# Kernel tuning notes

Hardware: AMD Instinct MI355X
Metric: run time of the kernel (lower is better)

Reference implementation:

```python
import jax, jax.numpy as jnp
import numpy as np

STATE_LEN = 128
SEQ_LEN = 2048  # middle segment length; total T = SEQ_LEN + 2*STATE_LEN = 2304


def _l2norm(t):
    # matches torch F.normalize(p=2, dim=-1, eps=1e-12)
    n = jnp.sqrt(jnp.sum(t * t, axis=-1, keepdims=True))
    return t / jnp.maximum(n, 1e-12)


def setup_inputs() -> dict:
    key = jax.random.key(0)
    ks = jax.random.split(key, 8)
    B, D, H, dk, dv = 1, 1024, 16, 64, 64
    T = SEQ_LEN + 2 * STATE_LEN
    x = jax.random.normal(ks[0], (B, T, D), dtype=jnp.float32)
    w = lambda k, do: jax.random.normal(k, (H, D, do), dtype=jnp.float32) * 0.02
    return {
        "x": x,
        "Wq": w(ks[1], dk),
        "Wk": w(ks[2], dk),
        "Wv": w(ks[3], dv),
        "Wq_state": w(ks[4], dk),
        "Wk_state": w(ks[5], dk),
        "Wv_state": w(ks[6], dv),
        "scaling_factor": jnp.full((H,), 1.0 / np.sqrt(dk), dtype=jnp.float32),
    }


def reference(x, Wq, Wk, Wv, Wq_state, Wk_state, Wv_state, scaling_factor):
    sl, seq = STATE_LEN, SEQ_LEN
    # extract_state: [start_state | sequence | end_state]
    x0 = x[:, :sl]
    xm = x[:, sl:sl + seq]
    x1 = x[:, sl + seq:]

    proj = lambda t, W: jnp.einsum('bsd,hdk->bhsk', t, W)  # StackedLinear, no bias

    q = jnp.concatenate([_l2norm(proj(x0, Wq_state)), _l2norm(proj(xm, Wq)), _l2norm(proj(x1, Wq_state))], axis=2)
    k = jnp.concatenate([_l2norm(proj(x0, Wk_state)), _l2norm(proj(xm, Wk)), _l2norm(proj(x1, Wk_state))], axis=2)
    v = jnp.concatenate([_l2norm(proj(x0, Wv_state)), _l2norm(proj(xm, Wv)), _l2norm(proj(x1, Wv_state))], axis=2)

    T = q.shape[2]
    row = jnp.arange(T)[:, None]
    col = jnp.arange(T)[None, :]
    allowed = col <= row  # causal (tril, diagonal=0)
    # end-state rows may not attend to start-state cols (attn_bias[..., seq+sl:seq+2sl, :sl] = 0 before log)
    allowed = allowed & ~((row >= sl + seq) & (col < sl))
    mask = jnp.where(allowed, 0.0, -jnp.inf).astype(q.dtype)  # log of 0/1 tril

    # per-head learnable scale applied to q@k^T, then additive mask, softmax, @v
    scores = jnp.einsum('bhqd,bhkd->bhqk', q, k) * scaling_factor[None, :, None, None] + mask
    att = jax.nn.softmax(scores, axis=-1)
    return jnp.einsum('bhqk,bhkd->bhqd', att, v)
```

## Files before the change

kernel.cpp:

```cpp
#include <hip/hip_runtime.h>
#include <hip/hip_bf16.h>

#define T_TOT 2304
#define DDIM  1024
#define NH    16
#define DK    64
#define SLEN  128
#define SEQ   2048

typedef __bf16 bf16x8 __attribute__((ext_vector_type(8)));
typedef __bf16 bf16x4 __attribute__((ext_vector_type(4)));
typedef float  f32x4  __attribute__((ext_vector_type(4)));

__device__ __forceinline__ void async_copy16(const void* gsrc, void* ldst) {
  __builtin_amdgcn_global_load_lds(
      (const __attribute__((address_space(1))) void*)gsrc,
      (__attribute__((address_space(3))) void*)ldst, 16, 0, 0);
}

__device__ __forceinline__ void lds_barrier() {
  __asm__ volatile("s_waitcnt lgkmcnt(0)\n\ts_barrier" ::: "memory");
}

__global__ __launch_bounds__(256) void convert_kernel(
    const float* __restrict__ x,
    const float* __restrict__ Wq, const float* __restrict__ Wk,
    const float* __restrict__ Wv, const float* __restrict__ Wqs,
    const float* __restrict__ Wks, const float* __restrict__ Wvs,
    __bf16* __restrict__ xb, __bf16* __restrict__ Wt) {
  const int b = blockIdx.x;
  const int tid = threadIdx.x;
  if (b < 576) {
    const float4* xin = (const float4*)x;
#pragma unroll
    for (int it = 0; it < 4; ++it) {
      int idx4 = b * 1024 + it * 256 + tid;
      float4 v = xin[idx4];
      bf16x4 o;
      o[0] = (__bf16)v.x; o[1] = (__bf16)v.y; o[2] = (__bf16)v.z; o[3] = (__bf16)v.w;
      *(bf16x4*)(xb + (size_t)idx4 * 4) = o;
    }
    return;
  }
  __shared__ float tile[64 * 65];
  const int wb = b - 576;
  const int m  = wb >> 8;
  const int rem = wb & 255;
  const int h  = rem >> 4;
  const int dt = rem & 15;
  const int d0 = dt * 64;
  const float* Wsrc = (m == 0 ? Wq : m == 1 ? Wk : m == 2 ? Wv
                      : m == 3 ? Wqs : m == 4 ? Wks : Wvs) + (size_t)h * (DDIM * DK);
#pragma unroll
  for (int rr = 0; rr < 4; ++rr) {
    int drow = rr * 16 + (tid >> 4);
    int nc   = (tid & 15) * 4;
    float4 v = *(const float4*)(Wsrc + (size_t)(d0 + drow) * DK + nc);
    tile[(nc + 0) * 65 + drow] = v.x;
    tile[(nc + 1) * 65 + drow] = v.y;
    tile[(nc + 2) * 65 + drow] = v.z;
    tile[(nc + 3) * 65 + drow] = v.w;
  }
  __syncthreads();
  {
    int n  = tid >> 2;
    int rg = (tid & 3) * 16;
    __bf16* dst = Wt + (((size_t)(m * NH + h)) * DK + n) * DDIM + d0 + rg;
    bf16x8 o0, o1;
#pragma unroll
    for (int e = 0; e < 8; e++) o0[e] = (__bf16)tile[n * 65 + rg + e];
#pragma unroll
    for (int e = 0; e < 8; e++) o1[e] = (__bf16)tile[n * 65 + rg + 8 + e];
    *(bf16x8*)dst = o0;
    *(bf16x8*)(dst + 8) = o1;
  }
}

__global__ __launch_bounds__(256) void proj_kernel(
    const __bf16* __restrict__ xb, const __bf16* __restrict__ Wt,
    const float* __restrict__ scal,
    __bf16* __restrict__ qkv, __bf16* __restrict__ vt) {
  const int ntile = blockIdx.x;
  const int rt    = blockIdx.y;
  const int which = blockIdx.z;
  const int r0    = rt * 64;
  const int m     = (rt < 2 || rt >= 34) ? which + 3 : which;

  __shared__ __bf16 Xs[64 * 64];
  __shared__ __bf16 Wsh[128 * 64];

  const int tid  = threadIdx.x;
  const int wave = tid >> 6, lane = tid & 63;
  const int quad = lane >> 4, lc = lane & 15;
  const int wr   = wave >> 1, wc = wave & 1;
  const int h    = ntile * 2 + wc;

  const __bf16* Wbase = Wt + ((size_t)m * NH) * (DK * DDIM) + (size_t)(ntile * 128) * DDIM;

  const f32x4 fz = {0.f, 0.f, 0.f, 0.f};
  f32x4 acc[2][4];
#pragma unroll
  for (int i = 0; i < 2; i++)
#pragma unroll
    for (int j = 0; j < 4; j++) acc[i][j] = fz;

  for (int k0 = 0; k0 < DDIM; k0 += 64) {
#pragma unroll
    for (int it = 0; it < 2; ++it) {
      int L = it * 256 + tid;
      int row = L >> 3, c = (L & 7) ^ (row & 7);
      async_copy16(xb + (size_t)(r0 + row) * DDIM + k0 + c * 8,
                   (char*)Xs + (size_t)(it * 256 + wave * 64) * 16);
    }
#pragma unroll
    for (int it = 0; it < 4; ++it) {
      int L = it * 256 + tid;
      int row = L >> 3, c = (L & 7) ^ (row & 7);
      async_copy16(Wbase + (size_t)row * DDIM + k0 + c * 8,
                   (char*)Wsh + (size_t)(it * 256 + wave * 64) * 16);
    }
    __syncthreads();
#pragma unroll
    for (int kk = 0; kk < 2; kk++) {
      bf16x8 afr[2], bfr[4];
#pragma unroll
      for (int i = 0; i < 2; i++) {
        int row = wr * 32 + i * 16 + lc;
        int ch  = (kk * 4 + quad) ^ (row & 7);
        afr[i] = *(const bf16x8*)(Xs + (row * 8 + ch) * 8);
      }
#pragma unroll
      for (int j = 0; j < 4; j++) {
        int row = wc * 64 + j * 16 + lc;
        int ch  = (kk * 4 + quad) ^ (row & 7);
        bfr[j] = *(const bf16x8*)(Wsh + (row * 8 + ch) * 8);
      }
#pragma unroll
      for (int i = 0; i < 2; i++)
#pragma unroll
        for (int j = 0; j < 4; j++)
          acc[i][j] = __builtin_amdgcn_mfma_f32_16x16x32_bf16(afr[i], bfr[j], acc[i][j], 0, 0, 0);
    }
    __syncthreads();
  }

  const float qscale = (which == 0) ? scal[h] * 1.44269504088896f : 1.0f;
  float inv4[2][4];
#pragma unroll
  for (int i = 0; i < 2; i++) {
#pragma unroll
    for (int r = 0; r < 4; r++) {
      float s = 0.f;
#pragma unroll
      for (int j = 0; j < 4; j++) { float v = acc[i][j][r]; s += v * v; }
#pragma unroll
      for (int off = 1; off < 16; off <<= 1) s += __shfl_xor(s, off, 64);
      inv4[i][r] = qscale / fmaxf(sqrtf(s), 1e-12f);
    }
  }
  if (which == 2) {
    __bf16* vtp = vt + (size_t)h * (DK * T_TOT);
#pragma unroll
    for (int i = 0; i < 2; i++) {
      int rowbase = r0 + wr * 32 + i * 16 + quad * 4;
#pragma unroll
      for (int j = 0; j < 4; j++) {
        bf16x4 o;
#pragma unroll
        for (int r = 0; r < 4; r++) o[r] = (__bf16)(acc[i][j][r] * inv4[i][r]);
        *(bf16x4*)(vtp + (size_t)(j * 16 + lc) * T_TOT + rowbase) = o;
      }
    }
  } else {
    __bf16* outp = qkv + ((size_t)(which * NH + h)) * ((size_t)T_TOT * DK);
#pragma unroll
    for (int i = 0; i < 2; i++)
#pragma unroll
      for (int r = 0; r < 4; r++) {
        int row = r0 + wr * 32 + i * 16 + quad * 4 + r;
#pragma unroll
        for (int j = 0; j < 4; j++)
          outp[(size_t)row * DK + j * 16 + lc] = (__bf16)(acc[i][j][r] * inv4[i][r]);
      }
  }
}

__global__ __launch_bounds__(256, 3) void attn_kernel(
    const __bf16* __restrict__ qkv, const __bf16* __restrict__ vt,
    float* __restrict__ Opart, float* __restrict__ Lpart) {
  const int b    = blockIdx.x;
  const int h    = b & 15;
  const int rest = b >> 4;
  const int qg   = 35 - (rest >> 1);
  const int si   = rest & 1;
  const int q0b  = qg * 64;
  const int tid  = threadIdx.x;
  const int wave = tid >> 6, lane = tid & 63;
  const int quad = lane >> 4, lc = lane & 15;

  const __bf16* qp = qkv + ((size_t)h) * ((size_t)T_TOT * DK);
  const __bf16* kp = qkv + ((size_t)(NH + h)) * ((size_t)T_TOT * DK);
  const __bf16* vp = vt + (size_t)h * (DK * T_TOT);

  __shared__ __align__(16) char smem[40960];
  __bf16* Ks = (__bf16*)smem;
  __bf16* Vs = (__bf16*)(smem + 16384);
  __bf16* Pw = (__bf16*)(smem + 32768) + wave * 1024;

  bf16x8 qf[2];
#pragma unroll
  for (int kk = 0; kk < 2; kk++)
    qf[kk] = *(const bf16x8*)(qp + (size_t)(q0b + wave * 16 + lc) * DK + kk * 32 + quad * 8);

  const f32x4 fz = {0.f, 0.f, 0.f, 0.f};
  f32x4 acc[4];
#pragma unroll
  for (int dt = 0; dt < 4; dt++) acc[dt] = fz;
  float lp = 0.f;

  const int jsAll = (q0b >= SLEN + SEQ) ? 2 : 0;
  const int n     = qg - jsAll + 1;
  const int half  = (n + 1) >> 1;
  const int j0    = jsAll + (si ? half : 0);
  const int j1    = si ? qg : (jsAll + half - 1);

  auto stage = [&](int j, int bufi) {
    const __bf16* kT = kp + (size_t)j * 64 * DK;
    __bf16* Kd = Ks + bufi * 4096;
    __bf16* Vd = Vs + bufi * 4096;
#pragma unroll
    for (int it = 0; it < 2; ++it) {
      int L = it * 256 + tid;
      int row = L >> 3, c = (L & 7) ^ (row & 7);
      async_copy16(kT + (size_t)row * DK + c * 8,
                   (char*)Kd + (size_t)(it * 256 + wave * 64) * 16);
    }
#pragma unroll
    for (int it = 0; it < 2; ++it) {
      int L = it * 256 + tid;
      int d = L >> 3, c = (L & 7) ^ (d & 7);
      async_copy16(vp + (size_t)d * T_TOT + j * 64 + c * 8,
                   (char*)Vd + (size_t)(it * 256 + wave * 64) * 16);
    }
  };

  int cur = 0;
  if (j0 <= j1) stage(j0, 0);

  for (int j = j0; j <= j1; ++j) {
    __syncthreads();
    if (j < j1) stage(j + 1, cur ^ 1);

    const __bf16* Kc = Ks + cur * 4096;
    const __bf16* Vc = Vs + cur * 4096;

    f32x4 s[4];
#pragma unroll
    for (int kvt = 0; kvt < 4; kvt++) {
      int row = kvt * 16 + lc;
      bf16x8 a0 = *(const bf16x8*)(Kc + (row * 8 + (quad ^ (lc & 7))) * 8);
      bf16x8 a1 = *(const bf16x8*)(Kc + (row * 8 + ((4 + quad) ^ (lc & 7))) * 8);
      f32x4 t = __builtin_amdgcn_mfma_f32_16x16x32_bf16(a0, qf[0], fz, 0, 0, 0);
      s[kvt]  = __builtin_amdgcn_mfma_f32_16x16x32_bf16(a1, qf[1], t, 0, 0, 0);
    }

    const bool diag = (j == qg);
#pragma unroll
    for (int kvt = 0; kvt < 4; kvt++) {
      if (diag) {
#pragma unroll
        for (int r = 0; r < 4; r++)
          if ((kvt * 16 + quad * 4 + r) > (wave * 16 + lc)) s[kvt][r] = -__builtin_inff();
      }
      bf16x4 pb;
#pragma unroll
      for (int r = 0; r < 4; r++) {
        float pe = exp2f(s[kvt][r]);
        lp += pe;
        pb[r] = (__bf16)pe;
      }
      int c = (kvt * 4 + quad) ^ ((lc & 7) << 1);
      *(bf16x4*)(Pw + lc * 64 + c * 4) = pb;
    }

    bf16x8 pB[2];
#pragma unroll
    for (int kk = 0; kk < 2; kk++)
      pB[kk] = *(const bf16x8*)(Pw + lc * 64 + ((kk * 8 + quad * 2) ^ ((lc & 7) << 1)) * 4);
#pragma unroll
    for (int dt = 0; dt < 4; dt++) {
      int row = dt * 16 + lc;
#pragma unroll
      for (int kk = 0; kk < 2; kk++) {
        bf16x8 vA = *(const bf16x8*)(Vc + (row * 8 + ((kk * 4 + quad) ^ (lc & 7))) * 8);
        acc[dt] = __builtin_amdgcn_mfma_f32_16x16x32_bf16(vA, pB[kk], acc[dt], 0, 0, 0);
      }
    }
    cur ^= 1;
  }

  lp += __shfl_xor(lp, 16, 64);
  lp += __shfl_xor(lp, 32, 64);
  if (lane < 16) Lpart[(size_t)b * 64 + wave * 16 + lane] = lp;

  __syncthreads();
  float* Ot = (float*)smem + wave * (16 * 68);
#pragma unroll
  for (int dt = 0; dt < 4; dt++)
#pragma unroll
    for (int r = 0; r < 4; r++)
      Ot[lc * 68 + dt * 16 + quad * 4 + r] = acc[dt][r];

  float* Ob = Opart + (size_t)b * 4096;
  const int q2 = lane >> 2, dsg = (lane & 3) * 16;
#pragma unroll
  for (int g = 0; g < 4; g++) {
    f32x4 v = *(const f32x4*)(&Ot[q2 * 68 + dsg + g * 4]);
    *(f32x4*)(&Ob[(size_t)(wave * 16 + q2) * 64 + dsg + g * 4]) = v;
  }
}

__global__ __launch_bounds__(256) void combine_kernel(
    const float* __restrict__ Opart, const float* __restrict__ Lpart,
    float* __restrict__ out) {
  const int b  = blockIdx.x;
  const int h  = b & 15;
  const int qg = b >> 4;
  const int b0 = (((35 - qg) * 2) << 4) | h;
  const int b1 = b0 + 16;
  const int tid = threadIdx.x;

  __shared__ float invl[64];
  if (tid < 64)
    invl[tid] = 1.0f / (Lpart[(size_t)b0 * 64 + tid] + Lpart[(size_t)b1 * 64 + tid]);
  __syncthreads();

  const float* O0 = Opart + (size_t)b0 * 4096;
  const float* O1 = Opart + (size_t)b1 * 4096;
  float* op = out + ((size_t)h * T_TOT + qg * 64) * DK;
#pragma unroll
  for (int it = 0; it < 4; ++it) {
    int i4 = it * 256 + tid;
    f32x4 a = *(const f32x4*)(&O0[i4 * 4]);
    f32x4 c = *(const f32x4*)(&O1[i4 * 4]);
    float iv = invl[i4 >> 4];
    f32x4 o;
#pragma unroll
    for (int r = 0; r < 4; r++) o[r] = (a[r] + c[r]) * iv;
    *(f32x4*)(&op[i4 * 4]) = o;
  }
}

extern "C" void kernel_launch(void* const* d_in, const int* in_sizes, int n_in,
                              void* d_out, int out_size, void* d_ws, size_t ws_size,
                              hipStream_t stream) {
  const float* x    = (const float*)d_in[0];
  const float* Wq   = (const float*)d_in[1];
  const float* Wk   = (const float*)d_in[2];
  const float* Wv   = (const float*)d_in[3];
  const float* Wqs  = (const float*)d_in[4];
  const float* Wks  = (const float*)d_in[5];
  const float* Wvs  = (const float*)d_in[6];
  const float* scal = (const float*)d_in[7];
  float* out = (float*)d_out;

  char* ws = (char*)d_ws;
  size_t off = 0;
  __bf16* xb    = (__bf16*)(ws + off); off += (size_t)T_TOT * DDIM * 2;
  __bf16* Wt    = (__bf16*)(ws + off); off += (size_t)6 * NH * DK * DDIM * 2;
  __bf16* qkv   = (__bf16*)(ws + off); off += (size_t)2 * NH * T_TOT * DK * 2;
  __bf16* vt    = (__bf16*)(ws + off); off += (size_t)NH * DK * T_TOT * 2;
  float*  Opart = (float*)(ws + off);  off += (size_t)1152 * 4096 * 4;
  float*  Lpart = (float*)(ws + off);

  convert_kernel<<<2112, 256, 0, stream>>>(x, Wq, Wk, Wv, Wqs, Wks, Wvs, xb, Wt);
  proj_kernel<<<dim3(8, 36, 3), 256, 0, stream>>>(xb, Wt, scal, qkv, vt);
  attn_kernel<<<dim3(1152), 256, 0, stream>>>(qkv, vt, Opart, Lpart);
  combine_kernel<<<dim3(576), 256, 0, stream>>>(Opart, Lpart, out);
}
```

Measured before the change: 142.1 us.

## Load projection GEMM operands directly from global memory into registers, dropping LDS staging

The projection kernel stops staging X and W tiles in shared memory through async copies and barriers. Each lane now loads its MFMA fragments straight from global memory into registers, and the k-loop is unrolled by two. This removes LDS traffic and block-wide synchronisation. In exchange, operands shared across waves are fetched redundantly from global memory or cache, and the reads are less coalesced.

```diff
diff --git a/kernel.cpp b/kernel.cpp
--- a/kernel.cpp
+++ b/kernel.cpp
@@ -16,10 +16,6 @@
   __builtin_amdgcn_global_load_lds(
       (const __attribute__((address_space(1))) void*)gsrc,
       (__attribute__((address_space(3))) void*)ldst, 16, 0, 0);
-}
-
-__device__ __forceinline__ void lds_barrier() {
-  __asm__ volatile("s_waitcnt lgkmcnt(0)\n\ts_barrier" ::: "memory");
 }
 
 __global__ __launch_bounds__(256) void convert_kernel(
@@ -86,16 +82,19 @@
   const int r0    = rt * 64;
   const int m     = (rt < 2 || rt >= 34) ? which + 3 : which;
 
-  __shared__ __bf16 Xs[64 * 64];
-  __shared__ __bf16 Wsh[128 * 64];
-
   const int tid  = threadIdx.x;
   const int wave = tid >> 6, lane = tid & 63;
   const int quad = lane >> 4, lc = lane & 15;
   const int wr   = wave >> 1, wc = wave & 1;
   const int h    = ntile * 2 + wc;
 
-  const __bf16* Wbase = Wt + ((size_t)m * NH) * (DK * DDIM) + (size_t)(ntile * 128) * DDIM;
+  const __bf16* xb0 = xb + (size_t)(r0 + wr * 32 + lc) * DDIM + quad * 8;
+  const __bf16* xb1 = xb0 + 16 * DDIM;
+  const __bf16* wb0 = Wt + ((size_t)m * NH) * (DK * DDIM)
+                    + (size_t)(ntile * 128 + wc * 64 + lc) * DDIM + quad * 8;
+  const __bf16* wb1 = wb0 + 16 * DDIM;
+  const __bf16* wb2 = wb0 + 32 * DDIM;
+  const __bf16* wb3 = wb0 + 48 * DDIM;
 
   const f32x4 fz = {0.f, 0.f, 0.f, 0.f};
   f32x4 acc[2][4];
@@ -104,44 +103,25 @@
 #pragma unroll
     for (int j = 0; j < 4; j++) acc[i][j] = fz;
 
+#pragma unroll 2
   for (int k0 = 0; k0 < DDIM; k0 += 64) {
-#pragma unroll
-    for (int it = 0; it < 2; ++it) {
-      int L = it * 256 + tid;
-      int row = L >> 3, c = (L & 7) ^ (row & 7);
-      async_copy16(xb + (size_t)(r0 + row) * DDIM + k0 + c * 8,
-                   (char*)Xs + (size_t)(it * 256 + wave * 64) * 16);
-    }
-#pragma unroll
-    for (int it = 0; it < 4; ++it) {
-      int L = it * 256 + tid;
-      int row = L >> 3, c = (L & 7) ^ (row & 7);
-      async_copy16(Wbase + (size_t)row * DDIM + k0 + c * 8,
-                   (char*)Wsh + (size_t)(it * 256 + wave * 64) * 16);
-    }
-    __syncthreads();
+    bf16x8 afr[2][2], bfr[4][2];
 #pragma unroll
     for (int kk = 0; kk < 2; kk++) {
-      bf16x8 afr[2], bfr[4];
-#pragma unroll
-      for (int i = 0; i < 2; i++) {
-        int row = wr * 32 + i * 16 + lc;
-        int ch  = (kk * 4 + quad) ^ (row & 7);
-        afr[i] = *(const bf16x8*)(Xs + (row * 8 + ch) * 8);
-      }
-#pragma unroll
-      for (int j = 0; j < 4; j++) {
-        int row = wc * 64 + j * 16 + lc;
-        int ch  = (kk * 4 + quad) ^ (row & 7);
-        bfr[j] = *(const bf16x8*)(Wsh + (row * 8 + ch) * 8);
-      }
+      afr[0][kk] = *(const bf16x8*)(xb0 + k0 + kk * 32);
+      afr[1][kk] = *(const bf16x8*)(xb1 + k0 + kk * 32);
+      bfr[0][kk] = *(const bf16x8*)(wb0 + k0 + kk * 32);
+      bfr[1][kk] = *(const bf16x8*)(wb1 + k0 + kk * 32);
+      bfr[2][kk] = *(const bf16x8*)(wb2 + k0 + kk * 32);
+      bfr[3][kk] = *(const bf16x8*)(wb3 + k0 + kk * 32);
+    }
+#pragma unroll
+    for (int kk = 0; kk < 2; kk++)
 #pragma unroll
       for (int i = 0; i < 2; i++)
 #pragma unroll
         for (int j = 0; j < 4; j++)
-          acc[i][j] = __builtin_amdgcn_mfma_f32_16x16x32_bf16(afr[i], bfr[j], acc[i][j], 0, 0, 0);
-    }
-    __syncthreads();
+          acc[i][j] = __builtin_amdgcn_mfma_f32_16x16x32_bf16(afr[i][kk], bfr[j][kk], acc[i][j], 0, 0, 0);
   }
 
   const float qscale = (which == 0) ? scal[h] * 1.44269504088896f : 1.0f;
```

New measurement: 209.8 us. 47.7% more time.

## Process 128-query tiles per block with three-way KV split in attention

Applied to the files above, without the earlier changes.

The attention kernel now handles 128 query rows per block, with each wave owning two 16-row query subtiles. Each staged K/V tile in LDS is therefore reused across twice as many queries, and the KV range is split three ways instead of two. The combine kernel now sums three partials, and waves whose rows lie entirely before a KV tile skip its compute. This raises register use and LDS to 48KB per block under the launch bound of 3, and the causal-diagonal blocks do more masked work.

```diff
diff --git a/kernel.cpp b/kernel.cpp
--- a/kernel.cpp
+++ b/kernel.cpp
@@ -16,10 +16,6 @@
   __builtin_amdgcn_global_load_lds(
       (const __attribute__((address_space(1))) void*)gsrc,
       (__attribute__((address_space(3))) void*)ldst, 16, 0, 0);
-}
-
-__device__ __forceinline__ void lds_barrier() {
-  __asm__ volatile("s_waitcnt lgkmcnt(0)\n\ts_barrier" ::: "memory");
 }
 
 __global__ __launch_bounds__(256) void convert_kernel(
@@ -189,11 +185,11 @@
     const __bf16* __restrict__ qkv, const __bf16* __restrict__ vt,
     float* __restrict__ Opart, float* __restrict__ Lpart) {
   const int b    = blockIdx.x;
-  const int h    = b & 15;
-  const int rest = b >> 4;
-  const int qg   = 35 - (rest >> 1);
-  const int si   = rest & 1;
-  const int q0b  = qg * 64;
+  const int qg2  = 17 - (b / 48);
+  const int r48  = b % 48;
+  const int si   = r48 >> 4;
+  const int h    = r48 & 15;
+  const int q0b  = qg2 * 128;
   const int tid  = threadIdx.x;
   const int wave = tid >> 6, lane = tid & 63;
   const int quad = lane >> 4, lc = lane & 15;
@@ -202,27 +198,31 @@
   const __bf16* kp = qkv + ((size_t)(NH + h)) * ((size_t)T_TOT * DK);
   const __bf16* vp = vt + (size_t)h * (DK * T_TOT);
 
-  __shared__ __align__(16) char smem[40960];
+  __shared__ __align__(16) char smem[49152];
   __bf16* Ks = (__bf16*)smem;
   __bf16* Vs = (__bf16*)(smem + 16384);
-  __bf16* Pw = (__bf16*)(smem + 32768) + wave * 1024;
-
-  bf16x8 qf[2];
-#pragma unroll
-  for (int kk = 0; kk < 2; kk++)
-    qf[kk] = *(const bf16x8*)(qp + (size_t)(q0b + wave * 16 + lc) * DK + kk * 32 + quad * 8);
+
+  bf16x8 qf[2][2];
+#pragma unroll
+  for (int qi = 0; qi < 2; qi++)
+#pragma unroll
+    for (int kk = 0; kk < 2; kk++)
+      qf[qi][kk] = *(const bf16x8*)(qp + (size_t)(q0b + wave * 32 + qi * 16 + lc) * DK + kk * 32 + quad * 8);
 
   const f32x4 fz = {0.f, 0.f, 0.f, 0.f};
-  f32x4 acc[4];
-#pragma unroll
-  for (int dt = 0; dt < 4; dt++) acc[dt] = fz;
-  float lp = 0.f;
-
-  const int jsAll = (q0b >= SLEN + SEQ) ? 2 : 0;
-  const int n     = qg - jsAll + 1;
-  const int half  = (n + 1) >> 1;
-  const int j0    = jsAll + (si ? half : 0);
-  const int j1    = si ? qg : (jsAll + half - 1);
+  f32x4 acc[2][4];
+#pragma unroll
+  for (int qi = 0; qi < 2; qi++)
+#pragma unroll
+    for (int dt = 0; dt < 4; dt++) acc[qi][dt] = fz;
+  float lp[2] = {0.f, 0.f};
+
+  const int js   = (qg2 == 17) ? 2 : 0;
+  const int jmax = 2 * qg2 + 1;
+  const int n    = jmax - js + 1;
+  const int base = n / 3, rem = n % 3;
+  const int j0   = js + si * base + (si < rem ? si : rem);
+  const int j1   = j0 + base + (si < rem ? 1 : 0) - 1;
 
   auto stage = [&](int j, int bufi) {
     const __bf16* kT = kp + (size_t)j * 64 * DK;
@@ -251,103 +251,129 @@
     __syncthreads();
     if (j < j1) stage(j + 1, cur ^ 1);
 
-    const __bf16* Kc = Ks + cur * 4096;
-    const __bf16* Vc = Vs + cur * 4096;
-
-    f32x4 s[4];
-#pragma unroll
-    for (int kvt = 0; kvt < 4; kvt++) {
-      int row = kvt * 16 + lc;
-      bf16x8 a0 = *(const bf16x8*)(Kc + (row * 8 + (quad ^ (lc & 7))) * 8);
-      bf16x8 a1 = *(const bf16x8*)(Kc + (row * 8 + ((4 + quad) ^ (lc & 7))) * 8);
-      f32x4 t = __builtin_amdgcn_mfma_f32_16x16x32_bf16(a0, qf[0], fz, 0, 0, 0);
-      s[kvt]  = __builtin_amdgcn_mfma_f32_16x16x32_bf16(a1, qf[1], t, 0, 0, 0);
-    }
-
-    const bool diag = (j == qg);
-#pragma unroll
-    for (int kvt = 0; kvt < 4; kvt++) {
-      if (diag) {
-#pragma unroll
-        for (int r = 0; r < 4; r++)
-          if ((kvt * 16 + quad * 4 + r) > (wave * 16 + lc)) s[kvt][r] = -__builtin_inff();
-      }
-      bf16x4 pb;
-#pragma unroll
-      for (int r = 0; r < 4; r++) {
-        float pe = exp2f(s[kvt][r]);
-        lp += pe;
-        pb[r] = (__bf16)pe;
-      }
-      int c = (kvt * 4 + quad) ^ ((lc & 7) << 1);
-      *(bf16x4*)(Pw + lc * 64 + c * 4) = pb;
-    }
-
-    bf16x8 pB[2];
-#pragma unroll
-    for (int kk = 0; kk < 2; kk++)
-      pB[kk] = *(const bf16x8*)(Pw + lc * 64 + ((kk * 8 + quad * 2) ^ ((lc & 7) << 1)) * 4);
-#pragma unroll
-    for (int dt = 0; dt < 4; dt++) {
-      int row = dt * 16 + lc;
-#pragma unroll
-      for (int kk = 0; kk < 2; kk++) {
-        bf16x8 vA = *(const bf16x8*)(Vc + (row * 8 + ((kk * 4 + quad) ^ (lc & 7))) * 8);
-        acc[dt] = __builtin_amdgcn_mfma_f32_16x16x32_bf16(vA, pB[kk], acc[dt], 0, 0, 0);
+    if (64 * j <= q0b + wave * 32 + 31) {
+      const __bf16* Kc = Ks + cur * 4096;
+      const __bf16* Vc = Vs + cur * 4096;
+
+      f32x4 s[4][2];
+#pragma unroll
+      for (int kvt = 0; kvt < 4; kvt++) {
+        int row = kvt * 16 + lc;
+        bf16x8 a0 = *(const bf16x8*)(Kc + (row * 8 + (quad ^ (lc & 7))) * 8);
+        bf16x8 a1 = *(const bf16x8*)(Kc + (row * 8 + ((4 + quad) ^ (lc & 7))) * 8);
+#pragma unroll
+        for (int qi = 0; qi < 2; qi++) {
+          f32x4 t = __builtin_amdgcn_mfma_f32_16x16x32_bf16(a0, qf[qi][0], fz, 0, 0, 0);
+          s[kvt][qi] = __builtin_amdgcn_mfma_f32_16x16x32_bf16(a1, qf[qi][1], t, 0, 0, 0);
+        }
+      }
+
+      const bool diagw = (64 * j + 63 > q0b + wave * 32);
+#pragma unroll
+      for (int qi = 0; qi < 2; qi++) {
+        __bf16* Pw = (__bf16*)(smem + 32768) + (wave * 2 + qi) * 1024;
+#pragma unroll
+        for (int kvt = 0; kvt < 4; kvt++) {
+          if (diagw) {
+#pragma unroll
+            for (int r = 0; r < 4; r++)
+              if (64 * j + kvt * 16 + quad * 4 + r > q0b + wave * 32 + qi * 16 + lc)
+                s[kvt][qi][r] = -__builtin_inff();
+          }
+          bf16x4 pb;
+#pragma unroll
+          for (int r = 0; r < 4; r++) {
+            float pe = exp2f(s[kvt][qi][r]);
+            lp[qi] += pe;
+            pb[r] = (__bf16)pe;
+          }
+          int c = (kvt * 4 + quad) ^ ((lc & 7) << 1);
+          *(bf16x4*)(Pw + lc * 64 + c * 4) = pb;
+        }
+      }
+
+      bf16x8 pB[2][2];
+#pragma unroll
+      for (int qi = 0; qi < 2; qi++) {
+        const __bf16* Pw = (const __bf16*)(smem + 32768) + (wave * 2 + qi) * 1024;
+#pragma unroll
+        for (int kk = 0; kk < 2; kk++)
+          pB[qi][kk] = *(const bf16x8*)(Pw + lc * 64 + ((kk * 8 + quad * 2) ^ ((lc & 7) << 1)) * 4);
+      }
+#pragma unroll
+      for (int dt = 0; dt < 4; dt++) {
+        int row = dt * 16 + lc;
+#pragma unroll
+        for (int kk = 0; kk < 2; kk++) {
+          bf16x8 vA = *(const bf16x8*)(Vc + (row * 8 + ((kk * 4 + quad) ^ (lc & 7))) * 8);
+#pragma unroll
+          for (int qi = 0; qi < 2; qi++)
+            acc[qi][dt] = __builtin_amdgcn_mfma_f32_16x16x32_bf16(vA, pB[qi][kk], acc[qi][dt], 0, 0, 0);
+        }
       }
     }
     cur ^= 1;
   }
 
-  lp += __shfl_xor(lp, 16, 64);
-  lp += __shfl_xor(lp, 32, 64);
-  if (lane < 16) Lpart[(size_t)b * 64 + wave * 16 + lane] = lp;
+#pragma unroll
+  for (int qi = 0; qi < 2; qi++) {
+    lp[qi] += __shfl_xor(lp[qi], 16, 64);
+    lp[qi] += __shfl_xor(lp[qi], 32, 64);
+  }
+  if (lane < 16) {
+    Lpart[(size_t)b * 128 + wave * 32 + lane]      = lp[0];
+    Lpart[(size_t)b * 128 + wave * 32 + 16 + lane] = lp[1];
+  }
 
   __syncthreads();
   float* Ot = (float*)smem + wave * (16 * 68);
-#pragma unroll
-  for (int dt = 0; dt < 4; dt++)
-#pragma unroll
-    for (int r = 0; r < 4; r++)
-      Ot[lc * 68 + dt * 16 + quad * 4 + r] = acc[dt][r];
-
-  float* Ob = Opart + (size_t)b * 4096;
+  float* Ob = Opart + (size_t)b * 8192;
   const int q2 = lane >> 2, dsg = (lane & 3) * 16;
 #pragma unroll
-  for (int g = 0; g < 4; g++) {
-    f32x4 v = *(const f32x4*)(&Ot[q2 * 68 + dsg + g * 4]);
-    *(f32x4*)(&Ob[(size_t)(wave * 16 + q2) * 64 + dsg + g * 4]) = v;
+  for (int qi = 0; qi < 2; qi++) {
+#pragma unroll
+    for (int dt = 0; dt < 4; dt++)
+#pragma unroll
+      for (int r = 0; r < 4; r++)
+        Ot[lc * 68 + dt * 16 + quad * 4 + r] = acc[qi][dt][r];
+#pragma unroll
+    for (int g = 0; g < 4; g++) {
+      f32x4 v = *(const f32x4*)(&Ot[q2 * 68 + dsg + g * 4]);
+      *(f32x4*)(&Ob[(size_t)(wave * 32 + qi * 16 + q2) * 64 + dsg + g * 4]) = v;
+    }
   }
 }
 
 __global__ __launch_bounds__(256) void combine_kernel(
     const float* __restrict__ Opart, const float* __restrict__ Lpart,
     float* __restrict__ out) {
-  const int b  = blockIdx.x;
-  const int h  = b & 15;
-  const int qg = b >> 4;
-  const int b0 = (((35 - qg) * 2) << 4) | h;
-  const int b1 = b0 + 16;
+  const int b   = blockIdx.x;
+  const int h   = b & 15;
+  const int qg2 = b >> 4;
+  const int bb  = (17 - qg2) * 48 + h;
   const int tid = threadIdx.x;
 
-  __shared__ float invl[64];
-  if (tid < 64)
-    invl[tid] = 1.0f / (Lpart[(size_t)b0 * 64 + tid] + Lpart[(size_t)b1 * 64 + tid]);
+  __shared__ float invl[128];
+  const float* L0 = Lpart + (size_t)bb * 128;
+  if (tid < 128)
+    invl[tid] = 1.0f / (L0[tid] + L0[16 * 128 + tid] + L0[32 * 128 + tid]);
   __syncthreads();
 
-  const float* O0 = Opart + (size_t)b0 * 4096;
-  const float* O1 = Opart + (size_t)b1 * 4096;
-  float* op = out + ((size_t)h * T_TOT + qg * 64) * DK;
-#pragma unroll
-  for (int it = 0; it < 4; ++it) {
+  const float* O0 = Opart + (size_t)bb * 8192;
+  const float* O1 = O0 + (size_t)16 * 8192;
+  const float* O2 = O0 + (size_t)32 * 8192;
+  float* op = out + ((size_t)h * T_TOT + qg2 * 128) * DK;
+#pragma unroll
+  for (int it = 0; it < 8; ++it) {
     int i4 = it * 256 + tid;
-    f32x4 a = *(const f32x4*)(&O0[i4 * 4]);
-    f32x4 c = *(const f32x4*)(&O1[i4 * 4]);
+    f32x4 a = *(const f32x4*)(O0 + (size_t)i4 * 4);
+    f32x4 c = *(const f32x4*)(O1 + (size_t)i4 * 4);
+    f32x4 d = *(const f32x4*)(O2 + (size_t)i4 * 4);
     float iv = invl[i4 >> 4];
     f32x4 o;
 #pragma unroll
-    for (int r = 0; r < 4; r++) o[r] = (a[r] + c[r]) * iv;
-    *(f32x4*)(&op[i4 * 4]) = o;
+    for (int r = 0; r < 4; r++) o[r] = (a[r] + c[r] + d[r]) * iv;
+    *(f32x4*)(op + (size_t)i4 * 4) = o;
   }
 }
 
@@ -370,11 +396,11 @@
   __bf16* Wt    = (__bf16*)(ws + off); off += (size_t)6 * NH * DK * DDIM * 2;
   __bf16* qkv   = (__bf16*)(ws + off); off += (size_t)2 * NH * T_TOT * DK * 2;
   __bf16* vt    = (__bf16*)(ws + off); off += (size_t)NH * DK * T_TOT * 2;
-  float*  Opart = (float*)(ws + off);  off += (size_t)1152 * 4096 * 4;
-  float*  Lpart = (float*)(ws + off);
+  float*  Opart = (float*)(ws + off);  off += (size_t)864 * 8192 * 4;
+  float*  Lpart = (float*)(ws + off);  off += (size_t)864 * 128 * 4;
 
   convert_kernel<<<2112, 256, 0, stream>>>(x, Wq, Wk, Wv, Wqs, Wks, Wvs, xb, Wt);
   proj_kernel<<<dim3(8, 36, 3), 256, 0, stream>>>(xb, Wt, scal, qkv, vt);
-  attn_kernel<<<dim3(1152), 256, 0, stream>>>(qkv, vt, Opart, Lpart);
-  combine_kernel<<<dim3(576), 256, 0, stream>>>(Opart, Lpart, out);
-}
+  attn_kernel<<<dim3(864), 256, 0, stream>>>(qkv, vt, Opart, Lpart);
+  combine_kernel<<<dim3(288), 256, 0, stream>>>(Opart, Lpart, out);
+}
```

New measurement: 149.1 us. +4.9%, slower.

## Drop split-KV partitioning and fuse normalization into attention, removing combine kernel

Applied to the files above, without the earlier changes.

Each attention block now processes the full key range for its 64-query group instead of half, and normalizes its output directly in registers before writing to the final output. This removes the combine kernel launch and the round trip of partial outputs and row sums through global memory. In exchange, the grid halves to 576 blocks, and the longest blocks do about twice the serial work, which can worsen tail latency and reduce occupancy.

```diff
diff --git a/kernel.cpp b/kernel.cpp
--- a/kernel.cpp
+++ b/kernel.cpp
@@ -16,10 +16,6 @@
   __builtin_amdgcn_global_load_lds(
       (const __attribute__((address_space(1))) void*)gsrc,
       (__attribute__((address_space(3))) void*)ldst, 16, 0, 0);
-}
-
-__device__ __forceinline__ void lds_barrier() {
-  __asm__ volatile("s_waitcnt lgkmcnt(0)\n\ts_barrier" ::: "memory");
 }
 
 __global__ __launch_bounds__(256) void convert_kernel(
@@ -187,12 +183,10 @@
 
 __global__ __launch_bounds__(256, 3) void attn_kernel(
     const __bf16* __restrict__ qkv, const __bf16* __restrict__ vt,
-    float* __restrict__ Opart, float* __restrict__ Lpart) {
+    float* __restrict__ out) {
   const int b    = blockIdx.x;
   const int h    = b & 15;
-  const int rest = b >> 4;
-  const int qg   = 35 - (rest >> 1);
-  const int si   = rest & 1;
+  const int qg   = 35 - (b >> 4);
   const int q0b  = qg * 64;
   const int tid  = threadIdx.x;
   const int wave = tid >> 6, lane = tid & 63;
@@ -218,11 +212,8 @@
   for (int dt = 0; dt < 4; dt++) acc[dt] = fz;
   float lp = 0.f;
 
-  const int jsAll = (q0b >= SLEN + SEQ) ? 2 : 0;
-  const int n     = qg - jsAll + 1;
-  const int half  = (n + 1) >> 1;
-  const int j0    = jsAll + (si ? half : 0);
-  const int j1    = si ? qg : (jsAll + half - 1);
+  const int j0 = (q0b >= SLEN + SEQ) ? 2 : 0;
+  const int j1 = qg;
 
   auto stage = [&](int j, int bufi) {
     const __bf16* kT = kp + (size_t)j * 64 * DK;
@@ -245,7 +236,7 @@
   };
 
   int cur = 0;
-  if (j0 <= j1) stage(j0, 0);
+  stage(j0, 0);
 
   for (int j = j0; j <= j1; ++j) {
     __syncthreads();
@@ -301,7 +292,11 @@
 
   lp += __shfl_xor(lp, 16, 64);
   lp += __shfl_xor(lp, 32, 64);
-  if (lane < 16) Lpart[(size_t)b * 64 + wave * 16 + lane] = lp;
+  const float inv = 1.0f / lp;
+#pragma unroll
+  for (int dt = 0; dt < 4; dt++)
+#pragma unroll
+    for (int r = 0; r < 4; r++) acc[dt][r] *= inv;
 
   __syncthreads();
   float* Ot = (float*)smem + wave * (16 * 68);
@@ -311,43 +306,12 @@
     for (int r = 0; r < 4; r++)
       Ot[lc * 68 + dt * 16 + quad * 4 + r] = acc[dt][r];
 
-  float* Ob = Opart + (size_t)b * 4096;
+  float* op = out + ((size_t)h * T_TOT + q0b) * DK;
   const int q2 = lane >> 2, dsg = (lane & 3) * 16;
 #pragma unroll
   for (int g = 0; g < 4; g++) {
     f32x4 v = *(const f32x4*)(&Ot[q2 * 68 + dsg + g * 4]);
-    *(f32x4*)(&Ob[(size_t)(wave * 16 + q2) * 64 + dsg + g * 4]) = v;
-  }
-}
-
-__global__ __launch_bounds__(256) void combine_kernel(
-    const float* __restrict__ Opart, const float* __restrict__ Lpart,
-    float* __restrict__ out) {
-  const int b  = blockIdx.x;
-  const int h  = b & 15;
-  const int qg = b >> 4;
-  const int b0 = (((35 - qg) * 2) << 4) | h;
-  const int b1 = b0 + 16;
-  const int tid = threadIdx.x;
-
-  __shared__ float invl[64];
-  if (tid < 64)
-    invl[tid] = 1.0f / (Lpart[(size_t)b0 * 64 + tid] + Lpart[(size_t)b1 * 64 + tid]);
-  __syncthreads();
-
-  const float* O0 = Opart + (size_t)b0 * 4096;
-  const float* O1 = Opart + (size_t)b1 * 4096;
-  float* op = out + ((size_t)h * T_TOT + qg * 64) * DK;
-#pragma unroll
-  for (int it = 0; it < 4; ++it) {
-    int i4 = it * 256 + tid;
-    f32x4 a = *(const f32x4*)(&O0[i4 * 4]);
-    f32x4 c = *(const f32x4*)(&O1[i4 * 4]);
-    float iv = invl[i4 >> 4];
-    f32x4 o;
-#pragma unroll
-    for (int r = 0; r < 4; r++) o[r] = (a[r] + c[r]) * iv;
-    *(f32x4*)(&op[i4 * 4]) = o;
+    *(f32x4*)(&op[(size_t)(wave * 16 + q2) * 64 + dsg + g * 4]) = v;
   }
 }
 
@@ -370,11 +334,8 @@
   __bf16* Wt    = (__bf16*)(ws + off); off += (size_t)6 * NH * DK * DDIM * 2;
   __bf16* qkv   = (__bf16*)(ws + off); off += (size_t)2 * NH * T_TOT * DK * 2;
   __bf16* vt    = (__bf16*)(ws + off); off += (size_t)NH * DK * T_TOT * 2;
-  float*  Opart = (float*)(ws + off);  off += (size_t)1152 * 4096 * 4;
-  float*  Lpart = (float*)(ws + off);
 
   convert_kernel<<<2112, 256, 0, stream>>>(x, Wq, Wk, Wv, Wqs, Wks, Wvs, xb, Wt);
   proj_kernel<<<dim3(8, 36, 3), 256, 0, stream>>>(xb, Wt, scal, qkv, vt);
-  attn_kernel<<<dim3(1152), 256, 0, stream>>>(qkv, vt, Opart, Lpart);
-  combine_kernel<<<dim3(576), 256, 0, stream>>>(Opart, Lpart, out);
-}
+  attn_kernel<<<dim3(576), 256, 0, stream>>>(qkv, vt, out);
+}
```

Result: slower. 145.5 us (+2.4%).
